# Optimization experiments

Hardware: AMD Instinct MI355X
Metric: run time of the kernel (lower is better)

The kernel has to match this reference:

```python
import jax, jax.numpy as jnp
import numpy as np

N = 50000      # num nodes (spots)
E = 800000     # num edges before self-loops
IN = 3000      # input_dim (HVGs)
HID = 512      # hidden_dim
LAT = 30       # latent_dim
HEADS = 1
NEG_SLOPE = 0.2


def setup_inputs() -> dict:
    key = jax.random.key(0)
    ks = jax.random.split(key, 8)
    x = jax.random.normal(ks[0], (N, IN), jnp.float32)
    edge_index = jax.random.randint(ks[1], (2, E), 0, N)
    edge_attr = jax.random.uniform(ks[2], (E,), jnp.float32)
    # parameters (Xavier-ish scales)
    enc_w1 = jax.random.normal(ks[3], (HID, IN), jnp.float32) * (1.0 / np.sqrt(IN))
    enc_b1 = jnp.zeros((HID,), jnp.float32)
    gat_w = jax.random.normal(ks[4], (HID, HEADS * LAT), jnp.float32) * (1.0 / np.sqrt(HID))
    gat_att = jax.random.normal(ks[5], (HEADS, 2 * LAT), jnp.float32) * 0.1
    gat_b = jnp.zeros((LAT,), jnp.float32)
    dec_w1 = jax.random.normal(ks[6], (HID, LAT), jnp.float32) * (1.0 / np.sqrt(LAT))
    dec_b1 = jnp.zeros((HID,), jnp.float32)
    dec_b2 = jnp.zeros((IN,), jnp.float32)
    return dict(x=x, edge_index=edge_index, edge_attr=edge_attr,
                enc_w1=enc_w1, enc_b1=enc_b1, gat_w=gat_w, gat_att=gat_att,
                gat_b=gat_b, dec_w1=dec_w1, dec_b1=dec_b1, dec_b2=dec_b2)


def _gat_layer(h, src, dst, eattr, gat_w, gat_att, gat_b):
    """GAT layer: Eq.5-7, concat=False (mean over heads), multiplicative edge_attr."""
    xh = (h @ gat_w).reshape(N, HEADS, LAT)          # W h, per head
    x_i = xh[dst]                                     # target node feats (E+N, H, LAT)
    x_j = xh[src]                                     # source node feats
    att_i, att_j = gat_att[:, :LAT], gat_att[:, LAT:]
    # e_ij = LeakyReLU(a^T [Wh_i || Wh_j])
    alpha = jnp.einsum('ehc,hc->eh', x_i, att_i) + jnp.einsum('ehc,hc->eh', x_j, att_j)
    alpha = jax.nn.leaky_relu(alpha, NEG_SLOPE)
    alpha = alpha * eattr[:, None]                    # edge weight applied pre-softmax
    # segment softmax over incoming edges of each target node (self-loops ensure non-empty)
    amax = jax.ops.segment_max(alpha, dst, num_segments=N)
    alpha = jnp.exp(alpha - amax[dst])
    denom = jax.ops.segment_sum(alpha, dst, num_segments=N)
    alpha = alpha / (denom[dst] + 1e-16)
    # h'_i = sum_j alpha_ij * W h_j
    msg = x_j * alpha[:, :, None]                     # (E+N, H, LAT)
    out = jax.ops.segment_sum(msg, dst, num_segments=N)  # (N, H, LAT)
    return out.mean(axis=1) + gat_b                   # concat=False -> mean over heads


def reference(x, edge_index, edge_attr, enc_w1, enc_b1, gat_w, gat_att, gat_b,
              dec_w1, dec_b1, dec_b2):
    # add self-loops with fill_value=1.0
    loops = jnp.arange(N, dtype=edge_index.dtype)
    src = jnp.concatenate([edge_index[0], loops])
    dst = jnp.concatenate([edge_index[1], loops])
    eattr = jnp.concatenate([edge_attr, jnp.ones((N,), edge_attr.dtype)])

    # encoder: fc1 -> ELU -> GAT -> ELU
    h = jax.nn.elu(x @ enc_w1.T + enc_b1)
    z = jax.nn.elu(_gat_layer(h, src, dst, eattr, gat_w, gat_att, gat_b))

    # decoder: fc1 -> ELU -> tied fc2 (W^b = W^T, own bias)
    hd = jax.nn.elu(z @ dec_w1.T + dec_b1)
    x_recon = hd @ enc_w1 + dec_b2
    return (x_recon, z)
```

## Files before the change

kernel.cpp:

```cpp
#include <hip/hip_runtime.h>
#include <hip/hip_bf16.h>
#include <math.h>

#define N_NODES 50000
#define E_EDGES 800000
#define ET (E_EDGES + N_NODES)
#define IN_DIM 3000
#define HID 512
#define LAT 30
#define XH_STRIDE 32
#define NEG_SLOPE 0.2f
#define KPAD 3072
#define ENC_NT 94
#define DEC_NT 16
#define APLANE 1040

typedef __bf16 bfv8 __attribute__((ext_vector_type(8)));
typedef float f32x4 __attribute__((ext_vector_type(4)));

__device__ __forceinline__ float eluf(float x) { return x > 0.f ? x : expm1f(x); }

__global__ void k_init(unsigned* __restrict__ hist) {
    int gid = blockIdx.x * 256 + threadIdx.x;
    if (gid < N_NODES) hist[gid] = 0u;
}

__global__ void k_transpose_w(const float* __restrict__ w, float* __restrict__ wt) {
    int idx = blockIdx.x * 256 + threadIdx.x;
    if (idx < HID * LAT) {
        int j = idx / LAT, c = idx % LAT;
        wt[c * HID + j] = w[idx];
    }
}

__global__ void k_conv_w(const float* __restrict__ w, __bf16* __restrict__ w1b, __bf16* __restrict__ w1bt) {
    int idx = blockIdx.x * 256 + threadIdx.x;
    if (idx >= HID * KPAD) return;
    int j = idx / KPAD, k = idx - j * KPAD;
    float v = (k < IN_DIM) ? w[(size_t)j * IN_DIM + k] : 0.f;
    __bf16 b = (__bf16)v;
    w1b[(size_t)j * KPAD + k] = b;
    w1bt[(size_t)k * HID + j] = b;
}

__global__ __launch_bounds__(256)
void k_enc_gemm(const float* __restrict__ A, const __bf16* __restrict__ Bb,
                const float* __restrict__ bias, float* __restrict__ C) {
    __shared__ __bf16 As[2][4 * APLANE];
    __shared__ __bf16 Bs[3][4096];
    const int tid = threadIdx.x;
    const int lane = tid & 63, wv = tid >> 6;
    const int wr = wv >> 1, wc = wv & 1;
    const int l16 = lane & 15, lh = lane >> 4;
    const int p = ((int)blockIdx.y >> 2) * 8 + (int)blockIdx.x;
    if (p > 390) return;
    const int i0 = p * 128;
    const int c0 = ((int)blockIdx.y & 3) * 128;

    const int arow = tid >> 2, akc = tid & 3;
    const int r0 = i0 + arow, r1 = i0 + arow + 64;
    const float* apA = A + (size_t)(r0 < N_NODES ? r0 : N_NODES - 1) * IN_DIM + akc * 8;
    const float* apB = A + (size_t)(r1 < N_NODES ? r1 : N_NODES - 1) * IN_DIM + akc * 8;

    f32x4 acc[4][4] = {};
    float4 R0[4], R1[4];

    auto stageB = [&](int kt, int b) {
#pragma unroll
        for (int s = 0; s < 2; ++s) {
            int g = wv * 2 + s;
            int col = (g & 1) * 64 + lane;
            int ks = g >> 1;
            const __bf16* src = Bb + (size_t)(c0 + col) * KPAD + kt + ks * 8;
            __builtin_amdgcn_global_load_lds(
                (const __attribute__((address_space(1))) void*)src,
                (__attribute__((address_space(3))) void*)(&Bs[b][(size_t)g * 512]),
                16, 0, 0);
        }
    };
    auto loadA = [&](int kt, float4* R) {
        R[0] = R[1] = R[2] = R[3] = make_float4(0.f, 0.f, 0.f, 0.f);
        if (kt + akc * 8 < IN_DIM) {
            const float4* p0 = (const float4*)(apA + kt);
            R[0] = p0[0]; R[1] = p0[1];
            const float4* p1 = (const float4*)(apB + kt);
            R[2] = p1[0]; R[3] = p1[1];
        }
    };
    auto writeA = [&](const float4* R, int b) {
        bfv8 pk;
        pk[0] = (__bf16)R[0].x; pk[1] = (__bf16)R[0].y; pk[2] = (__bf16)R[0].z; pk[3] = (__bf16)R[0].w;
        pk[4] = (__bf16)R[1].x; pk[5] = (__bf16)R[1].y; pk[6] = (__bf16)R[1].z; pk[7] = (__bf16)R[1].w;
        *(bfv8*)&As[b][(size_t)akc * APLANE + arow * 8] = pk;
        pk[0] = (__bf16)R[2].x; pk[1] = (__bf16)R[2].y; pk[2] = (__bf16)R[2].z; pk[3] = (__bf16)R[2].w;
        pk[4] = (__bf16)R[3].x; pk[5] = (__bf16)R[3].y; pk[6] = (__bf16)R[3].z; pk[7] = (__bf16)R[3].w;
        *(bfv8*)&As[b][(size_t)akc * APLANE + (arow + 64) * 8] = pk;
    };
    auto mfmaStep = [&](int tb, int bb) {
        bfv8 af[4], bfr[4];
#pragma unroll
        for (int mi = 0; mi < 4; ++mi)
            af[mi] = *(const bfv8*)&As[tb][(size_t)lh * APLANE + (wr * 64 + mi * 16 + l16) * 8];
#pragma unroll
        for (int ni = 0; ni < 4; ++ni)
            bfr[ni] = *(const bfv8*)&Bs[bb][((size_t)lh * 128 + wc * 64 + ni * 16 + l16) * 8];
#pragma unroll
        for (int mi = 0; mi < 4; ++mi)
#pragma unroll
            for (int ni = 0; ni < 4; ++ni)
                acc[mi][ni] = __builtin_amdgcn_mfma_f32_16x16x32_bf16(af[mi], bfr[ni], acc[mi][ni], 0, 0, 0);
    };

    loadA(0, R0);
    stageB(0, 0);
    stageB(32, 1);
    loadA(32, R1);
    asm volatile("s_waitcnt vmcnt(8)" ::: "memory");
    __builtin_amdgcn_sched_barrier(0);
    writeA(R0, 0);
    asm volatile("s_waitcnt vmcnt(6) lgkmcnt(0)" ::: "memory");
    __builtin_amdgcn_s_barrier();
    __builtin_amdgcn_sched_barrier(0);

    for (int tt = 0; tt < ENC_NT; tt += 2) {
        {
            const int t = tt;
            const bool ld = (t + 2) < ENC_NT;
            if (ld) {
                loadA((t + 2) * 32, R0);
                stageB((t + 2) * 32, (t + 2) % 3);
            }
            mfmaStep(t & 1, t % 3);
            if (ld) asm volatile("s_waitcnt vmcnt(6)" ::: "memory");
            else    asm volatile("s_waitcnt vmcnt(0)" ::: "memory");
            __builtin_amdgcn_sched_barrier(0);
            writeA(R1, (t + 1) & 1);
            asm volatile("s_waitcnt lgkmcnt(0)" ::: "memory");
            __builtin_amdgcn_s_barrier();
            __builtin_amdgcn_sched_barrier(0);
        }
        {
            const int t = tt + 1;
            const bool ld = (t + 2) < ENC_NT;
            const bool wr1 = (t + 1) < ENC_NT;
            if (ld) {
                loadA((t + 2) * 32, R1);
                stageB((t + 2) * 32, (t + 2) % 3);
            }
            mfmaStep(t & 1, t % 3);
            if (wr1) {
                if (ld) asm volatile("s_waitcnt vmcnt(6)" ::: "memory");
                else    asm volatile("s_waitcnt vmcnt(0)" ::: "memory");
                __builtin_amdgcn_sched_barrier(0);
                writeA(R0, (t + 1) & 1);
                asm volatile("s_waitcnt lgkmcnt(0)" ::: "memory");
                __builtin_amdgcn_s_barrier();
                __builtin_amdgcn_sched_barrier(0);
            }
        }
    }

#pragma unroll
    for (int ni = 0; ni < 4; ++ni) {
        int col = c0 + wc * 64 + ni * 16 + l16;
        float bv = bias[col];
#pragma unroll
        for (int mi = 0; mi < 4; ++mi) {
            int row0 = i0 + wr * 64 + mi * 16 + lh * 4;
#pragma unroll
            for (int r = 0; r < 4; ++r) {
                int row = row0 + r;
                if (row < N_NODES)
                    C[(size_t)row * HID + col] = eluf(acc[mi][ni][r] + bv);
            }
        }
    }
}

__global__ __launch_bounds__(256)
void k_dec_gemm(const __bf16* __restrict__ Ab, const __bf16* __restrict__ Bt,
                const float* __restrict__ bias, float* __restrict__ C) {
    __shared__ __bf16 As[3][4096];
    __shared__ __bf16 Bs[3][4096];
    const int tid = threadIdx.x;
    const int lane = tid & 63, wv = tid >> 6;
    const int wr = wv >> 1, wc = wv & 1;
    const int l16 = lane & 15, lh = lane >> 4;
    const int p = ((int)blockIdx.y / 24) * 8 + (int)blockIdx.x;
    if (p > 390) return;
    const int i0 = p * 128;
    const int c0 = ((int)blockIdx.y % 24) * 128;

    f32x4 acc[4][4] = {};

    auto stage = [&](int kt, int b) {
#pragma unroll
        for (int s = 0; s < 2; ++s) {
            int g = wv * 2 + s;
            int ks = g >> 1;
            int rc = (g & 1) * 64 + lane;
            int row = i0 + rc; if (row >= N_NODES) row = N_NODES - 1;
            const __bf16* srcA = Ab + (size_t)row * HID + kt + ks * 8;
            __builtin_amdgcn_global_load_lds(
                (const __attribute__((address_space(1))) void*)srcA,
                (__attribute__((address_space(3))) void*)(&As[b][(size_t)g * 512]),
                16, 0, 0);
            const __bf16* srcB = Bt + (size_t)(c0 + rc) * HID + kt + ks * 8;
            __builtin_amdgcn_global_load_lds(
                (const __attribute__((address_space(1))) void*)srcB,
                (__attribute__((address_space(3))) void*)(&Bs[b][(size_t)g * 512]),
                16, 0, 0);
        }
    };

    stage(0, 0);
    stage(32, 1);
    asm volatile("s_waitcnt vmcnt(4) lgkmcnt(0)" ::: "memory");
    __builtin_amdgcn_s_barrier();
    __builtin_amdgcn_sched_barrier(0);

#pragma unroll 1
    for (int t = 0; t < DEC_NT; ++t) {
        const int bt = t % 3;
        if (t + 2 < DEC_NT) stage((t + 2) * 32, (t + 2) % 3);
        bfv8 af[4], bfr[4];
#pragma unroll
        for (int mi = 0; mi < 4; ++mi)
            af[mi] = *(const bfv8*)&As[bt][((size_t)lh * 128 + wr * 64 + mi * 16 + l16) * 8];
#pragma unroll
        for (int ni = 0; ni < 4; ++ni)
            bfr[ni] = *(const bfv8*)&Bs[bt][((size_t)lh * 128 + wc * 64 + ni * 16 + l16) * 8];
#pragma unroll
        for (int mi = 0; mi < 4; ++mi)
#pragma unroll
            for (int ni = 0; ni < 4; ++ni)
                acc[mi][ni] = __builtin_amdgcn_mfma_f32_16x16x32_bf16(af[mi], bfr[ni], acc[mi][ni], 0, 0, 0);
        if (t + 2 < DEC_NT) {
            asm volatile("s_waitcnt vmcnt(4) lgkmcnt(0)" ::: "memory");
        } else {
            asm volatile("s_waitcnt vmcnt(0) lgkmcnt(0)" ::: "memory");
        }
        __builtin_amdgcn_s_barrier();
        __builtin_amdgcn_sched_barrier(0);
    }

#pragma unroll
    for (int ni = 0; ni < 4; ++ni) {
        int col = c0 + wc * 64 + ni * 16 + l16;
        if (col >= IN_DIM) continue;
        float bv = bias[col];
#pragma unroll
        for (int mi = 0; mi < 4; ++mi) {
            int row0 = i0 + wr * 64 + mi * 16 + lh * 4;
#pragma unroll
            for (int r = 0; r < 4; ++r) {
                int row = row0 + r;
                if (row < N_NODES)
                    C[(size_t)row * IN_DIM + col] = acc[mi][ni][r] + bv;
            }
        }
    }
}

__global__ __launch_bounds__(256)
void k_gat_proj(const float* __restrict__ h, const float* __restrict__ gat_w,
                const float* __restrict__ gat_att,
                float* __restrict__ xh, float* __restrict__ si, float* __restrict__ sj) {
    __shared__ float gwl[HID * LAT];
    __shared__ float atl[2 * LAT];
    int tid = threadIdx.x;
    for (int i = tid; i < HID * LAT; i += 256) gwl[i] = gat_w[i];
    if (tid < 2 * LAT) atl[tid] = gat_att[tid];
    __syncthreads();
    int c = tid & 31;
    bool act = c < LAT;
    for (int it = 0; it < 16; ++it) {
        int n = blockIdx.x * 128 + it * 8 + (tid >> 5);
        if (n >= N_NODES) continue;
        float accv = 0.f;
        const float4* h4 = (const float4*)(h + (size_t)n * HID);
#pragma unroll 4
        for (int j4 = 0; j4 < HID / 4; ++j4) {
            float4 hv = h4[j4];
            if (act) {
                int b = j4 * 4 * LAT + c;
                accv = fmaf(hv.x, gwl[b], accv);
                accv = fmaf(hv.y, gwl[b + LAT], accv);
                accv = fmaf(hv.z, gwl[b + 2 * LAT], accv);
                accv = fmaf(hv.w, gwl[b + 3 * LAT], accv);
            }
        }
        float xhv = act ? accv : 0.f;
        xh[(size_t)n * XH_STRIDE + c] = xhv;
        float sip = act ? atl[c] * xhv : 0.f;
        float sjp = act ? atl[LAT + c] * xhv : 0.f;
#pragma unroll
        for (int off = 16; off > 0; off >>= 1) {
            sip += __shfl_down(sip, off, 32);
            sjp += __shfl_down(sjp, off, 32);
        }
        if (c == 0) { si[n] = sip; sj[n] = sjp; }
    }
}

__global__ void k_hist(const int* __restrict__ ei, unsigned* __restrict__ hist) {
    int e = blockIdx.x * 256 + threadIdx.x;
    if (e >= ET) return;
    int d = (e < E_EDGES) ? ei[E_EDGES + e] : (e - E_EDGES);
    atomicAdd(&hist[d], 1u);
}

__global__ __launch_bounds__(1024)
void k_scan(const unsigned* __restrict__ hist, unsigned* __restrict__ off, unsigned* __restrict__ cursor) {
    __shared__ unsigned part[1024];
    const int tid = threadIdx.x;
    const int b = tid * 49;
    const int e = (b + 49 < N_NODES) ? b + 49 : N_NODES;
    unsigned s = 0;
    for (int i = b; i < e; ++i) s += hist[i];
    part[tid] = s;
    __syncthreads();
    for (int d = 1; d < 1024; d <<= 1) {
        unsigned v = (tid >= d) ? part[tid - d] : 0u;
        __syncthreads();
        part[tid] += v;
        __syncthreads();
    }
    unsigned run = (tid > 0) ? part[tid - 1] : 0u;
    for (int i = b; i < e; ++i) {
        off[i] = run; cursor[i] = run;
        run += hist[i];
    }
    if (tid == 1023) off[N_NODES] = run;
}

__global__ void k_fill(const int* __restrict__ ei, const float* __restrict__ eattr,
                       unsigned* __restrict__ cursor, int* __restrict__ csr_src,
                       float* __restrict__ csr_w) {
    int e = blockIdx.x * 256 + threadIdx.x;
    if (e >= ET) return;
    int s, d; float w;
    if (e < E_EDGES) { s = ei[e]; d = ei[E_EDGES + e]; w = eattr[e]; }
    else { s = d = e - E_EDGES; w = 1.f; }
    unsigned pos = atomicAdd(&cursor[d], 1u);
    csr_src[pos] = s;
    csr_w[pos] = w;
}

__global__ __launch_bounds__(256)
void k_gat_agg(const unsigned* __restrict__ off, const int* __restrict__ csr_src,
               const float* __restrict__ csr_w, const float* __restrict__ si,
               const float* __restrict__ sj, const float* __restrict__ xh,
               const float* __restrict__ gat_b,
               float* __restrict__ zbuf, float* __restrict__ zout) {
    const int n = blockIdx.x * 4 + (threadIdx.x >> 6);
    if (n >= N_NODES) return;
    const int lane = threadIdx.x & 63;
    const int beg = (int)off[n], end = (int)off[n + 1];
    const float s_i = si[n];
    const int c = lane & 31;
    const int half = lane >> 5;

    float m = -1e30f;
    for (int j = beg + lane; j < end; j += 64) {
        int s = csr_src[j];
        float a = s_i + sj[s];
        a = a >= 0.f ? a : NEG_SLOPE * a;
        a *= csr_w[j];
        m = fmaxf(m, a);
    }
#pragma unroll
    for (int o = 32; o > 0; o >>= 1) m = fmaxf(m, __shfl_xor(m, o));

    float denom = 0.f, acc = 0.f;
    for (int base = beg; base < end; base += 64) {
        int j = base + lane;
        float v = 0.f; int s = 0;
        if (j < end) {
            s = csr_src[j];
            float a = s_i + sj[s];
            a = a >= 0.f ? a : NEG_SLOPE * a;
            a *= csr_w[j];
            v = __expf(a - m);
        }
        denom += v;
        int cnt = end - base; if (cnt > 64) cnt = 64;
        for (int q = 0; q < cnt; q += 2) {
            int src_lane = q + half;
            float vq = __shfl(v, src_lane);
            int sq = __shfl(s, src_lane);
            acc = fmaf(vq, xh[(size_t)sq * XH_STRIDE + c], acc);
        }
    }
#pragma unroll
    for (int o = 32; o > 0; o >>= 1) denom += __shfl_xor(denom, o);
    acc += __shfl_xor(acc, 32);

    if (lane < LAT) {
        float v = eluf(acc / (denom + 1e-16f) + gat_b[c]);
        zbuf[(size_t)n * XH_STRIDE + c] = v;
        zout[(size_t)n * LAT + c] = v;
    }
}

__global__ __launch_bounds__(256)
void k_dec1(const float* __restrict__ zbuf, const float* __restrict__ wt,
            const float* __restrict__ b, __bf16* __restrict__ hdb) {
    int gid = blockIdx.x * 256 + threadIdx.x;
    if (gid >= N_NODES * HID) return;
    int j = gid & (HID - 1);
    size_t i = (size_t)(gid >> 9);
    float acc = b[j];
#pragma unroll
    for (int c = 0; c < LAT; ++c)
        acc = fmaf(zbuf[i * XH_STRIDE + c], wt[c * HID + j], acc);
    hdb[gid] = (__bf16)eluf(acc);
}

extern "C" void kernel_launch(void* const* d_in, const int* in_sizes, int n_in,
                              void* d_out, int out_size, void* d_ws, size_t ws_size,
                              hipStream_t stream) {
    const float* x      = (const float*)d_in[0];
    const int*   ei     = (const int*)d_in[1];
    const float* eattr  = (const float*)d_in[2];
    const float* enc_w1 = (const float*)d_in[3];
    const float* enc_b1 = (const float*)d_in[4];
    const float* gat_w  = (const float*)d_in[5];
    const float* gat_att= (const float*)d_in[6];
    const float* gat_b  = (const float*)d_in[7];
    const float* dec_w1 = (const float*)d_in[8];
    const float* dec_b1 = (const float*)d_in[9];
    const float* dec_b2 = (const float*)d_in[10];

    float* out  = (float*)d_out;
    float* xrec = out;
    float* zout = out + (size_t)N_NODES * IN_DIM;

    float* ws = (float*)d_ws;
    float*    h       = ws;
    float*    xh      = ws + 25600000;
    float*    zbuf    = ws + 27200000;
    float*    si      = ws + 28800000;
    float*    sj      = ws + 28850000;
    float*    wt      = ws + 28900000;
    __bf16*   w1b     = (__bf16*)(ws + 28915360);
    __bf16*   w1bt    = (__bf16*)(ws + 29701792);
    unsigned* hist    = (unsigned*)(ws + 30488224);
    unsigned* csr_off = (unsigned*)(ws + 30538224);
    unsigned* cursor  = (unsigned*)(ws + 30588226);
    int*      csr_src = (int*)(ws + 30638226);
    float*    csr_w   = (float*)(ws + 31488226);
    __bf16*   hdb     = (__bf16*)h;

    (void)in_sizes; (void)n_in; (void)out_size; (void)ws_size;

    k_init<<<(N_NODES + 255) / 256, 256, 0, stream>>>(hist);
    k_transpose_w<<<(HID * LAT + 255) / 256, 256, 0, stream>>>(dec_w1, wt);
    k_conv_w<<<(HID * KPAD + 255) / 256, 256, 0, stream>>>(enc_w1, w1b, w1bt);
    k_hist<<<(ET + 255) / 256, 256, 0, stream>>>(ei, hist);

    {
        dim3 g(8, 196);
        k_enc_gemm<<<g, 256, 0, stream>>>(x, w1b, enc_b1, h);
    }

    k_scan<<<1, 1024, 0, stream>>>(hist, csr_off, cursor);
    k_fill<<<(ET + 255) / 256, 256, 0, stream>>>(ei, eattr, cursor, csr_src, csr_w);
    k_gat_proj<<<(N_NODES + 127) / 128, 256, 0, stream>>>(h, gat_w, gat_att, xh, si, sj);
    k_gat_agg<<<(N_NODES + 3) / 4, 256, 0, stream>>>(csr_off, csr_src, csr_w, si, sj, xh, gat_b, zbuf, zout);
    k_dec1<<<(N_NODES * HID + 255) / 256, 256, 0, stream>>>(zbuf, wt, dec_b1, hdb);

    {
        dim3 g(8, 1176);
        k_dec_gemm<<<g, 256, 0, stream>>>(hdb, w1bt, dec_b2, xrec);
    }
}
```

Baseline: 1.771 ms.

## Pre-convert x to bf16 and run encoder GEMM via generic async-LDS kernel

Adds a pass that converts the fp32 input matrix to padded bf16. When the workspace is large enough, the encoder GEMM then runs through a templated bf16 GEMM that stages both operands with global_load_lds, replacing the register-staged fp32-A path. The decoder GEMM is folded into the same template. This trades an extra full read of x plus a bf16 write and re-read for a simpler, more asynchronous GEMM main loop, and it depends on the workspace size check passing.

After: 1.877 ms. +6.0%, slower.

```diff
diff --git a/kernel.cpp b/kernel.cpp
--- a/kernel.cpp
+++ b/kernel.cpp
@@ -12,7 +12,6 @@
 #define NEG_SLOPE 0.2f
 #define KPAD 3072
 #define ENC_NT 94
-#define DEC_NT 16
 #define APLANE 1040
 
 typedef __bf16 bfv8 __attribute__((ext_vector_type(8)));
@@ -41,6 +40,112 @@
     __bf16 b = (__bf16)v;
     w1b[(size_t)j * KPAD + k] = b;
     w1bt[(size_t)k * HID + j] = b;
+}
+
+__global__ __launch_bounds__(256)
+void k_conv_x(const float* __restrict__ x, __bf16* __restrict__ xb) {
+    const int CHR = KPAD / 8;
+    const int total = N_NODES * CHR;
+    for (int idx = blockIdx.x * 256 + threadIdx.x; idx < total; idx += gridDim.x * 256) {
+        int row = idx / CHR, kc = idx - row * CHR;
+        bfv8 pk = {};
+        if (kc < IN_DIM / 8) {
+            const float4* p = (const float4*)(x + (size_t)row * IN_DIM + kc * 8);
+            float4 v0 = p[0], v1 = p[1];
+            pk[0] = (__bf16)v0.x; pk[1] = (__bf16)v0.y; pk[2] = (__bf16)v0.z; pk[3] = (__bf16)v0.w;
+            pk[4] = (__bf16)v1.x; pk[5] = (__bf16)v1.y; pk[6] = (__bf16)v1.z; pk[7] = (__bf16)v1.w;
+        }
+        *(bfv8*)(xb + (size_t)row * KPAD + kc * 8) = pk;
+    }
+}
+
+template<int CPB, int LDA, int LDB, int LDC, int NT, bool ELU, bool COLG>
+__global__ __launch_bounds__(256)
+void k_bgemm(const __bf16* __restrict__ Ab, const __bf16* __restrict__ Bt,
+             const float* __restrict__ bias, float* __restrict__ C) {
+    __shared__ __bf16 As[3][4096];
+    __shared__ __bf16 Bs[3][4096];
+    const int tid = threadIdx.x;
+    const int lane = tid & 63, wv = tid >> 6;
+    const int wr = wv >> 1, wc = wv & 1;
+    const int l16 = lane & 15, lh = lane >> 4;
+    const int p = ((int)blockIdx.y / CPB) * 8 + (int)blockIdx.x;
+    if (p > 390) return;
+    const int i0 = p * 128;
+    const int c0 = ((int)blockIdx.y % CPB) * 128;
+
+    f32x4 acc[4][4] = {};
+
+    auto stage = [&](int kt, int b) {
+#pragma unroll
+        for (int s = 0; s < 2; ++s) {
+            int g = wv * 2 + s;
+            int ks = g >> 1;
+            int rc = (g & 1) * 64 + lane;
+            int row = i0 + rc; if (row >= N_NODES) row = N_NODES - 1;
+            const __bf16* srcA = Ab + (size_t)row * LDA + kt + ks * 8;
+            __builtin_amdgcn_global_load_lds(
+                (const __attribute__((address_space(1))) void*)srcA,
+                (__attribute__((address_space(3))) void*)(&As[b][(size_t)g * 512]),
+                16, 0, 0);
+            const __bf16* srcB = Bt + (size_t)(c0 + rc) * LDB + kt + ks * 8;
+            __builtin_amdgcn_global_load_lds(
+                (const __attribute__((address_space(1))) void*)srcB,
+                (__attribute__((address_space(3))) void*)(&Bs[b][(size_t)g * 512]),
+                16, 0, 0);
+        }
+    };
+
+    stage(0, 0);
+    stage(32, 1);
+    asm volatile("s_waitcnt vmcnt(4) lgkmcnt(0)" ::: "memory");
+    __builtin_amdgcn_s_barrier();
+    __builtin_amdgcn_sched_barrier(0);
+
+#pragma unroll 1
+    for (int t = 0; t < NT; ++t) {
+        const int bt = t % 3;
+        if (t + 2 < NT) stage((t + 2) * 32, (t + 2) % 3);
+        bfv8 af[4], bfr[4];
+#pragma unroll
+        for (int mi = 0; mi < 4; ++mi)
+            af[mi] = *(const bfv8*)&As[bt][((size_t)lh * 128 + wr * 64 + mi * 16 + l16) * 8];
+#pragma unroll
+        for (int ni = 0; ni < 4; ++ni)
+            bfr[ni] = *(const bfv8*)&Bs[bt][((size_t)lh * 128 + wc * 64 + ni * 16 + l16) * 8];
+#pragma unroll
+        for (int mi = 0; mi < 4; ++mi)
+#pragma unroll
+            for (int ni = 0; ni < 4; ++ni)
+                acc[mi][ni] = __builtin_amdgcn_mfma_f32_16x16x32_bf16(af[mi], bfr[ni], acc[mi][ni], 0, 0, 0);
+        if (t + 2 < NT) {
+            asm volatile("s_waitcnt vmcnt(4) lgkmcnt(0)" ::: "memory");
+        } else {
+            asm volatile("s_waitcnt vmcnt(0) lgkmcnt(0)" ::: "memory");
+        }
+        __builtin_amdgcn_s_barrier();
+        __builtin_amdgcn_sched_barrier(0);
+    }
+
+#pragma unroll
+    for (int ni = 0; ni < 4; ++ni) {
+        int col = c0 + wc * 64 + ni * 16 + l16;
+        if (COLG && col >= LDC) continue;
+        float bv = bias[col];
+#pragma unroll
+        for (int mi = 0; mi < 4; ++mi) {
+            int row0 = i0 + wr * 64 + mi * 16 + lh * 4;
+#pragma unroll
+            for (int r = 0; r < 4; ++r) {
+                int row = row0 + r;
+                if (row < N_NODES) {
+                    float v = acc[mi][ni][r] + bv;
+                    if (ELU) v = eluf(v);
+                    C[(size_t)row * LDC + col] = v;
+                }
+            }
+        }
+    }
 }
 
 __global__ __launch_bounds__(256)
@@ -126,10 +231,7 @@
         {
             const int t = tt;
             const bool ld = (t + 2) < ENC_NT;
-            if (ld) {
-                loadA((t + 2) * 32, R0);
-                stageB((t + 2) * 32, (t + 2) % 3);
-            }
+            if (ld) { loadA((t + 2) * 32, R0); stageB((t + 2) * 32, (t + 2) % 3); }
             mfmaStep(t & 1, t % 3);
             if (ld) asm volatile("s_waitcnt vmcnt(6)" ::: "memory");
             else    asm volatile("s_waitcnt vmcnt(0)" ::: "memory");
@@ -142,13 +244,10 @@
         {
             const int t = tt + 1;
             const bool ld = (t + 2) < ENC_NT;
-            const bool wr1 = (t + 1) < ENC_NT;
-            if (ld) {
-                loadA((t + 2) * 32, R1);
-                stageB((t + 2) * 32, (t + 2) % 3);
-            }
+            const bool w1 = (t + 1) < ENC_NT;
+            if (ld) { loadA((t + 2) * 32, R1); stageB((t + 2) * 32, (t + 2) % 3); }
             mfmaStep(t & 1, t % 3);
-            if (wr1) {
+            if (w1) {
                 if (ld) asm volatile("s_waitcnt vmcnt(6)" ::: "memory");
                 else    asm volatile("s_waitcnt vmcnt(0)" ::: "memory");
                 __builtin_amdgcn_sched_barrier(0);
@@ -172,91 +271,6 @@
                 int row = row0 + r;
                 if (row < N_NODES)
                     C[(size_t)row * HID + col] = eluf(acc[mi][ni][r] + bv);
-            }
-        }
-    }
-}
-
-__global__ __launch_bounds__(256)
-void k_dec_gemm(const __bf16* __restrict__ Ab, const __bf16* __restrict__ Bt,
-                const float* __restrict__ bias, float* __restrict__ C) {
-    __shared__ __bf16 As[3][4096];
-    __shared__ __bf16 Bs[3][4096];
-    const int tid = threadIdx.x;
-    const int lane = tid & 63, wv = tid >> 6;
-    const int wr = wv >> 1, wc = wv & 1;
-    const int l16 = lane & 15, lh = lane >> 4;
-    const int p = ((int)blockIdx.y / 24) * 8 + (int)blockIdx.x;
-    if (p > 390) return;
-    const int i0 = p * 128;
-    const int c0 = ((int)blockIdx.y % 24) * 128;
-
-    f32x4 acc[4][4] = {};
-
-    auto stage = [&](int kt, int b) {
-#pragma unroll
-        for (int s = 0; s < 2; ++s) {
-            int g = wv * 2 + s;
-            int ks = g >> 1;
-            int rc = (g & 1) * 64 + lane;
-            int row = i0 + rc; if (row >= N_NODES) row = N_NODES - 1;
-            const __bf16* srcA = Ab + (size_t)row * HID + kt + ks * 8;
-            __builtin_amdgcn_global_load_lds(
-                (const __attribute__((address_space(1))) void*)srcA,
-                (__attribute__((address_space(3))) void*)(&As[b][(size_t)g * 512]),
-                16, 0, 0);
-            const __bf16* srcB = Bt + (size_t)(c0 + rc) * HID + kt + ks * 8;
-            __builtin_amdgcn_global_load_lds(
-                (const __attribute__((address_space(1))) void*)srcB,
-                (__attribute__((address_space(3))) void*)(&Bs[b][(size_t)g * 512]),
-                16, 0, 0);
-        }
-    };
-
-    stage(0, 0);
-    stage(32, 1);
-    asm volatile("s_waitcnt vmcnt(4) lgkmcnt(0)" ::: "memory");
-    __builtin_amdgcn_s_barrier();
-    __builtin_amdgcn_sched_barrier(0);
-
-#pragma unroll 1
-    for (int t = 0; t < DEC_NT; ++t) {
-        const int bt = t % 3;
-        if (t + 2 < DEC_NT) stage((t + 2) * 32, (t + 2) % 3);
-        bfv8 af[4], bfr[4];
-#pragma unroll
-        for (int mi = 0; mi < 4; ++mi)
-            af[mi] = *(const bfv8*)&As[bt][((size_t)lh * 128 + wr * 64 + mi * 16 + l16) * 8];
-#pragma unroll
-        for (int ni = 0; ni < 4; ++ni)
-            bfr[ni] = *(const bfv8*)&Bs[bt][((size_t)lh * 128 + wc * 64 + ni * 16 + l16) * 8];
-#pragma unroll
-        for (int mi = 0; mi < 4; ++mi)
-#pragma unroll
-            for (int ni = 0; ni < 4; ++ni)
-                acc[mi][ni] = __builtin_amdgcn_mfma_f32_16x16x32_bf16(af[mi], bfr[ni], acc[mi][ni], 0, 0, 0);
-        if (t + 2 < DEC_NT) {
-            asm volatile("s_waitcnt vmcnt(4) lgkmcnt(0)" ::: "memory");
-        } else {
-            asm volatile("s_waitcnt vmcnt(0) lgkmcnt(0)" ::: "memory");
-        }
-        __builtin_amdgcn_s_barrier();
-        __builtin_amdgcn_sched_barrier(0);
-    }
-
-#pragma unroll
-    for (int ni = 0; ni < 4; ++ni) {
-        int col = c0 + wc * 64 + ni * 16 + l16;
-        if (col >= IN_DIM) continue;
-        float bv = bias[col];
-#pragma unroll
-        for (int mi = 0; mi < 4; ++mi) {
-            int row0 = i0 + wr * 64 + mi * 16 + lh * 4;
-#pragma unroll
-            for (int r = 0; r < 4; ++r) {
-                int row = row0 + r;
-                if (row < N_NODES)
-                    C[(size_t)row * IN_DIM + col] = acc[mi][ni][r] + bv;
             }
         }
     }
@@ -450,16 +464,24 @@
     unsigned* cursor  = (unsigned*)(ws + 30588226);
     int*      csr_src = (int*)(ws + 30638226);
     float*    csr_w   = (float*)(ws + 31488226);
+    __bf16*   xb      = (__bf16*)(ws + 32338228);
     __bf16*   hdb     = (__bf16*)h;
 
-    (void)in_sizes; (void)n_in; (void)out_size; (void)ws_size;
+    (void)in_sizes; (void)n_in; (void)out_size;
+
+    const bool big_ws = ws_size >= 436553000ull;
 
     k_init<<<(N_NODES + 255) / 256, 256, 0, stream>>>(hist);
     k_transpose_w<<<(HID * LAT + 255) / 256, 256, 0, stream>>>(dec_w1, wt);
     k_conv_w<<<(HID * KPAD + 255) / 256, 256, 0, stream>>>(enc_w1, w1b, w1bt);
     k_hist<<<(ET + 255) / 256, 256, 0, stream>>>(ei, hist);
 
-    {
+    if (big_ws) {
+        k_conv_x<<<2048, 256, 0, stream>>>(x, xb);
+        dim3 g(8, 49 * 4);
+        k_bgemm<4, KPAD, KPAD, HID, KPAD / 32, true, false>
+            <<<g, 256, 0, stream>>>(xb, w1b, enc_b1, h);
+    } else {
         dim3 g(8, 196);
         k_enc_gemm<<<g, 256, 0, stream>>>(x, w1b, enc_b1, h);
     }
@@ -471,7 +493,8 @@
     k_dec1<<<(N_NODES * HID + 255) / 256, 256, 0, stream>>>(zbuf, wt, dec_b1, hdb);
 
     {
-        dim3 g(8, 1176);
-        k_dec_gemm<<<g, 256, 0, stream>>>(hdb, w1bt, dec_b2, xrec);
-    }
-}
+        dim3 g(8, 49 * 24);
+        k_bgemm<24, HID, HID, IN_DIM, HID / 32, false, true>
+            <<<g, 256, 0, stream>>>(hdb, w1bt, dec_b2, xrec);
+    }
+}
```
